# Kernel tuning notes

Hardware: AMD Instinct MI355X
Metric: run time of the kernel (lower is better)

## Reference

```python
import jax, jax.numpy as jnp
import numpy as np

N, DEG = 20000, 16
E = N * DEG
D_IN, D_HID, D_OUT, L = 1024, 512, 128, 3


def setup_inputs() -> dict:
    key = jax.random.key(0)
    ks = jax.random.split(key, 16)
    scale = 0.02
    X = jax.random.normal(ks[0], (N, D_IN), dtype=jnp.float32)
    senders = jax.random.randint(ks[1], (E,), 0, N)
    receivers = jnp.repeat(jnp.arange(N), DEG)  # sorted, every node has DEG neighbors
    inp = {"X": X, "senders": senders, "receivers": receivers}
    ki = 2
    for l in range(L):
        din = D_IN >> l
        dh = D_HID >> l
        inp[f"lw{l}"] = jax.random.normal(ks[ki], (2 * din, dh), jnp.float32) * scale; ki += 1
        inp[f"lb{l}"] = jnp.zeros((dh,), jnp.float32)
        inp[f"aw{l}"] = jax.random.normal(ks[ki], (din, dh), jnp.float32) * scale; ki += 1
        inp[f"aq{l}"] = jax.random.normal(ks[ki], (dh,), jnp.float32) * scale; ki += 1
    inp["ow"] = jax.random.normal(ks[ki], (D_HID >> (L - 1), D_OUT), jnp.float32) * scale
    inp["ob"] = jnp.zeros((D_OUT,), jnp.float32)
    return inp


def _attend(h, senders, receivers, aw, aq):
    # scores depend only on the neighbor (sender) embedding: q @ relu(W h_j)
    logits = jnp.einsum('nh,h->n', jax.nn.relu(h @ aw), aq)            # [N]
    el = logits[senders]                                               # [E]
    m = jax.ops.segment_max(el, receivers, num_segments=N)            # per-receiver max
    w = jnp.exp(el - m[receivers])                                     # [E]
    denom = jax.ops.segment_sum(w, receivers, num_segments=N)         # [N]
    msg = jax.ops.segment_sum(w[:, None] * h[senders], receivers, num_segments=N)  # [N,D]
    return msg / denom[:, None]


def reference(X, senders, receivers,
              lw0, lb0, aw0, aq0,
              lw1, lb1, aw1, aq1,
              lw2, lb2, aw2, aq2,
              ow, ob):
    params = [(lw0, lb0, aw0, aq0), (lw1, lb1, aw1, aq1), (lw2, lb2, aw2, aq2)]
    h = X
    for lw, lb, aw, aq in params:
        hN = _attend(h, senders, receivers, aw, aq)
        h = jax.nn.relu(jnp.concatenate([h, hN], axis=1) @ lw + lb)
    return h[14] @ ow + ob
```

## Files before the change

kernel.cpp:

```cpp
#include <hip/hip_runtime.h>
#include <math.h>

typedef unsigned short ushort_t;
typedef __attribute__((ext_vector_type(8))) short short8;
typedef __attribute__((ext_vector_type(4))) float f32x4;

#define NN    20000
#define DEG   16
constexpr int MAXL2 = 1 + DEG;
constexpr int MAXL1 = MAXL2 + MAXL2*DEG;
constexpr int MAXL0 = MAXL1*DEG;
constexpr int L0PAD = 73 * 64;
constexpr int NWBLK = 512;

__device__ __forceinline__ ushort_t f2bf(float f) {
    unsigned u = __float_as_uint(f);
    return (ushort_t)((u + 0x7FFFu + ((u >> 16) & 1u)) >> 16);
}

__global__ __launch_bounds__(256)
void k_frontier(const int* __restrict__ senders,
                int* list2, int* inv2, int* list1, int* inv1,
                int* list0, int* inv0, int* cnts, float4* zp, int n4) {
    int t = threadIdx.x;
    if (blockIdx.x > 0) {
        int i = (blockIdx.x - 1) * 256 + t;
        if (i < n4) zp[i] = make_float4(0.f, 0.f, 0.f, 0.f);
        return;
    }
    __shared__ unsigned bm[625];
    __shared__ int cnt;
    auto clear = [&]() { for (int i = t; i < 625; i += 256) bm[i] = 0u; if (t == 0) cnt = 0; };
    auto tryadd = [&](int node, int* list, int* inv) {
        unsigned bit = 1u << (node & 31);
        unsigned old = atomicOr(&bm[node >> 5], bit);
        if (!(old & bit)) { int p = atomicAdd(&cnt, 1); list[p] = node; inv[node] = p; }
    };
    clear(); __syncthreads();
    if (t < 17) { int node = (t < 16) ? senders[14 * DEG + t] : 14; tryadd(node, list2, inv2); }
    __syncthreads();
    int c2 = cnt; if (t == 0) cnts[2] = c2;
    __syncthreads(); clear(); __syncthreads();
    for (int i = t; i < c2 * 17; i += 256) {
        int r = i / 17, k = i - 17 * r;
        int node = (k < 16) ? senders[list2[r] * DEG + k] : list2[r];
        tryadd(node, list1, inv1);
    }
    __syncthreads();
    int c1 = cnt; if (t == 0) cnts[1] = c1;
    __syncthreads(); clear(); __syncthreads();
    for (int i = t; i < c1 * 16; i += 256) {
        int r = i >> 4, k = i & 15;
        tryadd(senders[list1[r] * DEG + k], list0, inv0);
    }
    __syncthreads();
    if (t == 0) cnts[0] = cnt;
}

__global__ __launch_bounds__(256)
void k_prep(const float* __restrict__ W, ushort_t* __restrict__ WT,
            const float* __restrict__ X, const int* __restrict__ list0,
            const int* __restrict__ cnt0, ushort_t* __restrict__ Xg) {
    int t = threadIdx.x;
    if (blockIdx.x < NWBLK) {
        __shared__ float tile[32][33];
        int b = blockIdx.x;
        int bx = b & 15, by = b >> 4;
        int i0 = t >> 3, j0 = (t & 7) * 4;
        int k = by * 32 + i0, n0 = bx * 32;
        float4 v = *(const float4*)(W + (size_t)k * 512 + n0 + j0);
        tile[i0][j0] = v.x; tile[i0][j0 + 1] = v.y; tile[i0][j0 + 2] = v.z; tile[i0][j0 + 3] = v.w;
        __syncthreads();
        int n = n0 + i0, kc = j0;
        ushort_t* p = WT + (size_t)n * 1024 + by * 32 + kc;
        p[0] = f2bf(tile[kc][i0]); p[1] = f2bf(tile[kc + 1][i0]);
        p[2] = f2bf(tile[kc + 2][i0]); p[3] = f2bf(tile[kc + 3][i0]);
    } else {
        int r = blockIdx.x - NWBLK;
        int rc = *cnt0;
        ushort_t o0 = 0, o1 = 0, o2 = 0, o3 = 0;
        if (r < rc) {
            float4 v = *(const float4*)(X + (size_t)list0[r] * 1024 + t * 4);
            o0 = f2bf(v.x); o1 = f2bf(v.y); o2 = f2bf(v.z); o3 = f2bf(v.w);
        }
        ushort_t* p = Xg + (size_t)r * 1024 + t * 4;
        p[0] = o0; p[1] = o1; p[2] = o2; p[3] = o3;
    }
}

__global__ __launch_bounds__(256)
void k_logits_mfma(const ushort_t* __restrict__ Xg,
                   const ushort_t* __restrict__ WT,
                   const float* __restrict__ aq, float* __restrict__ lgc,
                   const int* __restrict__ cnt, int K, int KS) {
    __shared__ short As[64 * 40];
    __shared__ short Bs[64 * 40];
    int rcnt = *cnt;
    int row0 = blockIdx.x * 64;
    if (row0 >= rcnt) return;
    int col0 = blockIdx.y * 64;
    int kbeg = blockIdx.z * KS, kend = kbeg + KS;
    int t = threadIdx.x;
    int w = t >> 6, lane = t & 63;

    int sr = t >> 2, sk = (t & 3) * 8;
    const ushort_t* ap = Xg + (size_t)(row0 + sr) * K + sk;
    const ushort_t* bp = WT + (size_t)(col0 + sr) * K + sk;

    int fm = lane & 15, fq = lane >> 4;
    const short* arow = As + (w * 16 + fm) * 40 + fq * 8;
    const short* brow = Bs + fm * 40 + fq * 8;

    f32x4 acc0 = {0.f,0.f,0.f,0.f}, acc1 = {0.f,0.f,0.f,0.f};
    f32x4 acc2 = {0.f,0.f,0.f,0.f}, acc3 = {0.f,0.f,0.f,0.f};

    short8 pa = *(const short8*)(ap + kbeg);
    short8 pb = *(const short8*)(bp + kbeg);
    for (int k0 = kbeg; k0 < kend; k0 += 32) {
        *(short8*)(As + sr * 40 + sk) = pa;
        *(short8*)(Bs + sr * 40 + sk) = pb;
        __syncthreads();
        if (k0 + 32 < kend) {
            pa = *(const short8*)(ap + k0 + 32);
            pb = *(const short8*)(bp + k0 + 32);
        }
        short8 af = *(const short8*)arow;
        short8 b0 = *(const short8*)(brow);
        short8 b1 = *(const short8*)(brow + 16 * 40);
        short8 b2 = *(const short8*)(brow + 32 * 40);
        short8 b3 = *(const short8*)(brow + 48 * 40);
        acc0 = __builtin_amdgcn_mfma_f32_16x16x32_bf16(af, b0, acc0, 0, 0, 0);
        acc1 = __builtin_amdgcn_mfma_f32_16x16x32_bf16(af, b1, acc1, 0, 0, 0);
        acc2 = __builtin_amdgcn_mfma_f32_16x16x32_bf16(af, b2, acc2, 0, 0, 0);
        acc3 = __builtin_amdgcn_mfma_f32_16x16x32_bf16(af, b3, acc3, 0, 0, 0);
        __syncthreads();
    }

    float aqv0 = aq[col0 + fm], aqv1 = aq[col0 + 16 + fm];
    float aqv2 = aq[col0 + 32 + fm], aqv3 = aq[col0 + 48 + fm];
#pragma unroll
    for (int r = 0; r < 4; r++) {
        float v = fmaxf(acc0[r], 0.f) * aqv0 + fmaxf(acc1[r], 0.f) * aqv1
                + fmaxf(acc2[r], 0.f) * aqv2 + fmaxf(acc3[r], 0.f) * aqv3;
#pragma unroll
        for (int off = 1; off < 16; off <<= 1) v += __shfl_xor(v, off);
        if (fm == 0) atomicAdd(&lgc[row0 + w * 16 + fq * 4 + r], v);
    }
}

__global__ __launch_bounds__(256)
void k_matmul(const float* __restrict__ A1, const float* __restrict__ A2,
              const int* __restrict__ list, const int* __restrict__ inv,
              const float* __restrict__ B, const float* __restrict__ aq,
              float* __restrict__ C, const int* __restrict__ cnt,
              int amode, int omode, int K1, int K2, int NC, int KS) {
    __shared__ float As[32][68];
    __shared__ float Bs[32][64];
    __shared__ float rowsum[64];

    int rcnt = *cnt;
    int row0 = blockIdx.x * 64;
    if (row0 >= rcnt) return;
    int col0 = blockIdx.y * 64;
    int K = K1 + K2;
    int kbeg = blockIdx.z * KS;
    int kend = kbeg + KS; if (kend > K) kend = K;

    int t = threadIdx.x;
    int ty = t >> 4, tx = t & 15;
    int lr = t >> 2, kaoff = (t & 3) * 4;
    int grow = row0 + lr;
    bool rowValid = grow < rcnt;
    const float* rp1 = A1;
    const float* rp2 = A2;
    if (rowValid) {
        int hrow;
        if (amode == 0) hrow = grow;
        else { int node = list[grow]; hrow = (amode == 2) ? inv[node] : node; }
        rp1 = A1 + (size_t)hrow * K1;
        rp2 = A2 + (size_t)grow * K2;
    }
    const float* Bp = B + col0;
    int bidx0 = t, bidx1 = t + 256;

    auto loadA = [&](int k) -> float4 {
        if (!rowValid) return make_float4(0.f, 0.f, 0.f, 0.f);
        const float* src = (k < K1) ? (rp1 + k) : (rp2 + (k - K1));
        return *(const float4*)src;
    };
    auto loadB = [&](int idx, int k0) -> float4 {
        int row = idx >> 4, c4 = (idx & 15) * 4;
        return *(const float4*)(Bp + (size_t)(k0 + row) * NC + c4);
    };

    float4 pa0 = loadA(kbeg + kaoff);
    float4 pa1 = loadA(kbeg + kaoff + 16);
    float4 pb0 = loadB(bidx0, kbeg);
    float4 pb1 = loadB(bidx1, kbeg);

    float acc[4][4] = {};
    for (int k0 = kbeg; k0 < kend; k0 += 32) {
        As[kaoff + 0][lr] = pa0.x; As[kaoff + 1][lr] = pa0.y;
        As[kaoff + 2][lr] = pa0.z; As[kaoff + 3][lr] = pa0.w;
        As[kaoff + 16][lr] = pa1.x; As[kaoff + 17][lr] = pa1.y;
        As[kaoff + 18][lr] = pa1.z; As[kaoff + 19][lr] = pa1.w;
        *(float4*)&Bs[bidx0 >> 4][(bidx0 & 15) * 4] = pb0;
        *(float4*)&Bs[bidx1 >> 4][(bidx1 & 15) * 4] = pb1;
        __syncthreads();
        if (k0 + 32 < kend) {
            pa0 = loadA(k0 + 32 + kaoff);
            pa1 = loadA(k0 + 32 + kaoff + 16);
            pb0 = loadB(bidx0, k0 + 32);
            pb1 = loadB(bidx1, k0 + 32);
        }
#pragma unroll
        for (int kk = 0; kk < 32; kk++) {
            float4 a4 = *(const float4*)&As[kk][ty * 4];
            float4 b4 = *(const float4*)&Bs[kk][tx * 4];
            float a[4] = {a4.x, a4.y, a4.z, a4.w};
            float b[4] = {b4.x, b4.y, b4.z, b4.w};
#pragma unroll
            for (int i = 0; i < 4; i++)
#pragma unroll
                for (int j = 0; j < 4; j++) acc[i][j] += a[i] * b[j];
        }
        __syncthreads();
    }

    if (omode == 0) {
#pragma unroll
        for (int i = 0; i < 4; i++) {
            int r = row0 + ty * 4 + i;
            if (r < rcnt) {
                float* Crow = C + (size_t)r * NC + col0 + tx * 4;
#pragma unroll
                for (int j = 0; j < 4; j++) atomicAdd(&Crow[j], acc[i][j]);
            }
        }
    } else {
        if (t < 64) rowsum[t] = 0.f;
        __syncthreads();
        float aqv[4];
#pragma unroll
        for (int j = 0; j < 4; j++) aqv[j] = aq[col0 + tx * 4 + j];
#pragma unroll
        for (int i = 0; i < 4; i++) {
            float s = 0.f;
#pragma unroll
            for (int j = 0; j < 4; j++) {
                float v = acc[i][j];
                v = v > 0.f ? v : 0.f;
                s += v * aqv[j];
            }
            atomicAdd(&rowsum[ty * 4 + i], s);
        }
        __syncthreads();
        if (t < 64) {
            int r = row0 + t;
            if (r < rcnt) atomicAdd(&C[r], rowsum[t]);
        }
    }
}

__global__ void k_bias_relu(const float* __restrict__ C, const float* __restrict__ b,
                            float* __restrict__ H, const int* __restrict__ cnt, int ncShift) {
    int rcnt = *cnt;
    int NC = 1 << ncShift;
    int e = blockIdx.x * 256 + threadIdx.x;
    int r = e >> ncShift;
    if (r >= rcnt) return;
    int c = e & (NC - 1);
    float v = C[(size_t)r * NC + c] + b[c];
    H[(size_t)r * NC + c] = v > 0.f ? v : 0.f;
}

__global__ __launch_bounds__(256)
void k_agg(const float* __restrict__ Hsrc, const int* __restrict__ invH,
           const float* __restrict__ lgc, const int* __restrict__ invL,
           const int* __restrict__ senders,
           const int* __restrict__ listN, const int* __restrict__ cntN,
           float* __restrict__ hN, int din) {
    __shared__ int   s_row[DEG];
    __shared__ float s_w[DEG];
    __shared__ float s_scale;
    int b = blockIdx.x;
    if (b >= *cntN) return;
    int n = listN[b];
    int t = threadIdx.x;
    if (t < DEG) {
        int s = senders[n * DEG + t];
        s_row[t] = invH ? invH[s] : s;
        s_w[t] = lgc[invL ? invL[s] : s];
    }
    __syncthreads();
    if (t == 0) {
        float m = -1e30f;
        for (int k = 0; k < DEG; k++) m = fmaxf(m, s_w[k]);
        float d = 0.f;
        for (int k = 0; k < DEG; k++) { float w = expf(s_w[k] - m); s_w[k] = w; d += w; }
        s_scale = 1.f / d;
    }
    __syncthreads();
    float scale = s_scale;
    for (int dI = t; dI < din; dI += 256) {
        float acc = 0.f;
#pragma unroll
        for (int k = 0; k < DEG; k++)
            acc += s_w[k] * Hsrc[(size_t)s_row[k] * din + dI];
        hN[(size_t)b * din + dI] = acc * scale;
    }
}

__global__ __launch_bounds__(256)
void k_layer2(const float* __restrict__ h2c, const int* __restrict__ inv2,
              const int* __restrict__ senders,
              const float* __restrict__ aw2, const float* __restrict__ aq2,
              const float* __restrict__ lw2, const float* __restrict__ lb2,
              const float* __restrict__ ow, const float* __restrict__ ob,
              const int* __restrict__ cnt2, float* __restrict__ out) {
    __shared__ float h2s[17][256];
    __shared__ float pl[17][128];
    __shared__ float lg[17];
    __shared__ float wgt[16];
    __shared__ int   srow[16];
    __shared__ int   iv14s;
    __shared__ float hcat[512];
    __shared__ float h3[128];
    int t = threadIdx.x;
    int rc = *cnt2;
    for (int i = t; i < 17 * 256; i += 256) {
        int r = i >> 8, c = i & 255;
        h2s[r][c] = (r < rc) ? h2c[r * 256 + c] : 0.f;
    }
    if (t < 17) lg[t] = 0.f;
    if (t == 0) iv14s = inv2[14];
    __syncthreads();

    int c = t & 127, h = t >> 7;
    float acc[17];
#pragma unroll
    for (int i = 0; i < 17; i++) acc[i] = 0.f;
    for (int k4 = h * 32; k4 < h * 32 + 32; k4++) {
        int k = k4 * 4;
        float w0 = aw2[(size_t)k * 128 + c];
        float w1 = aw2[(size_t)(k + 1) * 128 + c];
        float w2 = aw2[(size_t)(k + 2) * 128 + c];
        float w3 = aw2[(size_t)(k + 3) * 128 + c];
#pragma unroll
        for (int r = 0; r < 17; r++) {
            float4 hv = *(const float4*)&h2s[r][k4 * 4];
            acc[r] += hv.x * w0 + hv.y * w1 + hv.z * w2 + hv.w * w3;
        }
    }
    if (h == 1) {
#pragma unroll
        for (int r = 0; r < 17; r++) pl[r][c] = acc[r];
    }
    __syncthreads();
    if (h == 0) {
        float aqv = aq2[c];
#pragma unroll
        for (int r = 0; r < 17; r++) {
            float v = acc[r] + pl[r][c];
            v = (v > 0.f ? v : 0.f) * aqv;
#pragma unroll
            for (int off = 1; off < 64; off <<= 1) v += __shfl_xor(v, off);
            if ((t & 63) == 0) atomicAdd(&lg[r], v);
        }
    }
    __syncthreads();
    if (t == 0) {
        float m = -1e30f; float l[16];
#pragma unroll
        for (int k = 0; k < 16; k++) {
            int s = senders[14 * DEG + k];
            int r = inv2[s];
            srow[k] = r; l[k] = lg[r];
            m = fmaxf(m, l[k]);
        }
        float d = 0.f;
#pragma unroll
        for (int k = 0; k < 16; k++) { float w = expf(l[k] - m); wgt[k] = w; d += w; }
        float invd = 1.f / d;
#pragma unroll
        for (int k = 0; k < 16; k++) wgt[k] *= invd;
    }
    __syncthreads();
    {
        float a = 0.f;
        int cc = t & 255;
        if (t < 256) {
#pragma unroll
            for (int k = 0; k < 16; k++) a += wgt[k] * h2s[srow[k]][cc];
            hcat[256 + cc] = a;
            hcat[cc] = h2s[iv14s][cc];
        }
    }
    __syncthreads();
    if (t < 128) {
        float a = lb2[t];
        for (int k = 0; k < 512; k++) a += hcat[k] * lw2[(size_t)k * 128 + t];
        h3[t] = a > 0.f ? a : 0.f;
    }
    __syncthreads();
    if (t < 128) {
        float a = ob[t];
        for (int k = 0; k < 128; k++) a += h3[k] * ow[(size_t)k * 128 + t];
        out[t] = a;
    }
}

extern "C" void kernel_launch(void* const* d_in, const int* in_sizes, int n_in,
                              void* d_out, int out_size, void* d_ws, size_t ws_size,
                              hipStream_t stream) {
    const float* X       = (const float*)d_in[0];
    const int*   senders = (const int*)d_in[1];
    const float* lw0 = (const float*)d_in[3];
    const float* lb0 = (const float*)d_in[4];
    const float* aw0 = (const float*)d_in[5];
    const float* aq0 = (const float*)d_in[6];
    const float* lw1 = (const float*)d_in[7];
    const float* lb1 = (const float*)d_in[8];
    const float* aw1 = (const float*)d_in[9];
    const float* aq1 = (const float*)d_in[10];
    const float* lw2 = (const float*)d_in[11];
    const float* lb2 = (const float*)d_in[12];
    const float* aw2 = (const float*)d_in[13];
    const float* aq2 = (const float*)d_in[14];
    const float* owp = (const float*)d_in[15];
    const float* obp = (const float*)d_in[16];
    float* out = (float*)d_out;

    char* ws = (char*)d_ws;
    size_t off = 0;
    auto alloc = [&](size_t nbytes) -> void* {
        void* p = ws + off;
        off += (nbytes + 255) & ~(size_t)255;
        return p;
    };
    float* lgc0 = (float*)alloc(L0PAD * 4);
    float* lgc1 = (float*)alloc(MAXL1 * 4);
    float* C0   = (float*)alloc((size_t)MAXL1 * 512 * 4);
    float* C1   = (float*)alloc((size_t)MAXL2 * 256 * 4);
    size_t zero_end = off;
    int* inv0  = (int*)alloc(NN * 4);
    int* inv1  = (int*)alloc(NN * 4);
    int* inv2  = (int*)alloc(NN * 4);
    int* list0 = (int*)alloc(L0PAD * 4);
    int* list1 = (int*)alloc(MAXL1 * 4);
    int* list2 = (int*)alloc(MAXL2 * 4);
    int* cnts  = (int*)alloc(4 * 4);
    ushort_t* Xg  = (ushort_t*)alloc((size_t)L0PAD * 1024 * 2);
    ushort_t* awT = (ushort_t*)alloc((size_t)512 * 1024 * 2);
    float* hN0c = (float*)alloc((size_t)MAXL1 * 1024 * 4);
    float* h1c  = (float*)alloc((size_t)MAXL1 * 512 * 4);
    float* hN1c = (float*)alloc((size_t)MAXL2 * 512 * 4);
    float* h2c  = (float*)alloc((size_t)MAXL2 * 256 * 4);
    (void)in_sizes; (void)n_in; (void)out_size; (void)ws_size;

    int nz4 = (int)(zero_end / 16);
    int nzb = (nz4 + 255) / 256;

    hipLaunchKernelGGL(k_frontier, dim3(1 + nzb), dim3(256), 0, stream,
                       senders, list2, inv2, list1, inv1, list0, inv0, cnts,
                       (float4*)ws, nz4);
    hipLaunchKernelGGL(k_prep, dim3(NWBLK + L0PAD), dim3(256), 0, stream,
                       aw0, awT, X, list0, cnts + 0, Xg);

    hipLaunchKernelGGL(k_logits_mfma, dim3(73, 512 / 64, 2), dim3(256), 0, stream,
                       Xg, awT, aq0, lgc0, cnts + 0, 1024, 512);
    hipLaunchKernelGGL(k_agg, dim3(MAXL1), dim3(256), 0, stream,
                       X, (const int*)nullptr, lgc0, inv0, senders, list1, cnts + 1, hN0c, 1024);
    hipLaunchKernelGGL(k_matmul, dim3((MAXL1 + 63) / 64, 512 / 64, 8), dim3(256), 0, stream,
                       X, hN0c, list1, (int*)nullptr, lw0, aq0, C0, cnts + 1,
                       1, 0, 1024, 1024, 512, 256);
    hipLaunchKernelGGL(k_bias_relu, dim3((MAXL1 * 512 + 255) / 256), dim3(256), 0, stream,
                       C0, lb0, h1c, cnts + 1, 9);

    hipLaunchKernelGGL(k_matmul, dim3((MAXL1 + 63) / 64, 256 / 64, 2), dim3(256), 0, stream,
                       h1c, h1c, list1, (int*)nullptr, aw1, aq1, lgc1, cnts + 1,
                       0, 1, 512, 0, 256, 256);
    hipLaunchKernelGGL(k_agg, dim3(MAXL2), dim3(256), 0, stream,
                       h1c, inv1, lgc1, inv1, senders, list2, cnts + 2, hN1c, 512);
    hipLaunchKernelGGL(k_matmul, dim3(1, 256 / 64, 8), dim3(256), 0, stream,
                       h1c, hN1c, list2, inv1, lw1, aq1, C1, cnts + 2,
                       2, 0, 512, 512, 256, 128);
    hipLaunchKernelGGL(k_bias_relu, dim3((MAXL2 * 256 + 255) / 256), dim3(256), 0, stream,
                       C1, lb1, h2c, cnts + 2, 8);

    hipLaunchKernelGGL(k_layer2, dim3(1), dim3(256), 0, stream,
                       h2c, inv2, senders, aw2, aq2, lw2, lb2, owp, obp, cnts + 2, out);
}
```

Measured before the change: 292.4 us.

## Replace single-block final layer with generic matmul/agg kernels and drop split-K

Replaces the monolithic one-block layer-2 kernel with the existing k_matmul and k_agg kernels, using a one-node list for the output row, plus a small k_out kernel for the output projection. It also removes split-K from the layer-0 logits MFMA kernel and from the layer-1 logits matmul. The intent is to spread the final-layer work over more blocks and to avoid the atomic accumulation of split-K on the logits. In exchange it adds three more kernel launches and gives the logits kernels fewer blocks.

Measured after the change: 284.1 us. -2.8%, faster.

```diff
diff --git a/kernel.cpp b/kernel.cpp
--- a/kernel.cpp
+++ b/kernel.cpp
@@ -21,7 +21,7 @@
 __global__ __launch_bounds__(256)
 void k_frontier(const int* __restrict__ senders,
                 int* list2, int* inv2, int* list1, int* inv1,
-                int* list0, int* inv0, int* cnts, float4* zp, int n4) {
+                int* list0, int* inv0, int* list3, int* cnts, float4* zp, int n4) {
     int t = threadIdx.x;
     if (blockIdx.x > 0) {
         int i = (blockIdx.x - 1) * 256 + t;
@@ -54,7 +54,7 @@
         tryadd(senders[list1[r] * DEG + k], list0, inv0);
     }
     __syncthreads();
-    if (t == 0) cnts[0] = cnt;
+    if (t == 0) { cnts[0] = cnt; cnts[3] = 1; list3[0] = 14; }
 }
 
 __global__ __launch_bounds__(256)
@@ -92,14 +92,13 @@
 void k_logits_mfma(const ushort_t* __restrict__ Xg,
                    const ushort_t* __restrict__ WT,
                    const float* __restrict__ aq, float* __restrict__ lgc,
-                   const int* __restrict__ cnt, int K, int KS) {
+                   const int* __restrict__ cnt, int K) {
     __shared__ short As[64 * 40];
     __shared__ short Bs[64 * 40];
     int rcnt = *cnt;
     int row0 = blockIdx.x * 64;
     if (row0 >= rcnt) return;
     int col0 = blockIdx.y * 64;
-    int kbeg = blockIdx.z * KS, kend = kbeg + KS;
     int t = threadIdx.x;
     int w = t >> 6, lane = t & 63;
 
@@ -114,13 +113,13 @@
     f32x4 acc0 = {0.f,0.f,0.f,0.f}, acc1 = {0.f,0.f,0.f,0.f};
     f32x4 acc2 = {0.f,0.f,0.f,0.f}, acc3 = {0.f,0.f,0.f,0.f};
 
-    short8 pa = *(const short8*)(ap + kbeg);
-    short8 pb = *(const short8*)(bp + kbeg);
-    for (int k0 = kbeg; k0 < kend; k0 += 32) {
+    short8 pa = *(const short8*)(ap);
+    short8 pb = *(const short8*)(bp);
+    for (int k0 = 0; k0 < K; k0 += 32) {
         *(short8*)(As + sr * 40 + sk) = pa;
         *(short8*)(Bs + sr * 40 + sk) = pb;
         __syncthreads();
-        if (k0 + 32 < kend) {
+        if (k0 + 32 < K) {
             pa = *(const short8*)(ap + k0 + 32);
             pb = *(const short8*)(bp + k0 + 32);
         }
@@ -311,103 +310,21 @@
     }
 }
 
-__global__ __launch_bounds__(256)
-void k_layer2(const float* __restrict__ h2c, const int* __restrict__ inv2,
-              const int* __restrict__ senders,
-              const float* __restrict__ aw2, const float* __restrict__ aq2,
-              const float* __restrict__ lw2, const float* __restrict__ lb2,
-              const float* __restrict__ ow, const float* __restrict__ ob,
-              const int* __restrict__ cnt2, float* __restrict__ out) {
-    __shared__ float h2s[17][256];
-    __shared__ float pl[17][128];
-    __shared__ float lg[17];
-    __shared__ float wgt[16];
-    __shared__ int   srow[16];
-    __shared__ int   iv14s;
-    __shared__ float hcat[512];
-    __shared__ float h3[128];
-    int t = threadIdx.x;
-    int rc = *cnt2;
-    for (int i = t; i < 17 * 256; i += 256) {
-        int r = i >> 8, c = i & 255;
-        h2s[r][c] = (r < rc) ? h2c[r * 256 + c] : 0.f;
-    }
-    if (t < 17) lg[t] = 0.f;
-    if (t == 0) iv14s = inv2[14];
-    __syncthreads();
-
-    int c = t & 127, h = t >> 7;
-    float acc[17];
-#pragma unroll
-    for (int i = 0; i < 17; i++) acc[i] = 0.f;
-    for (int k4 = h * 32; k4 < h * 32 + 32; k4++) {
-        int k = k4 * 4;
-        float w0 = aw2[(size_t)k * 128 + c];
-        float w1 = aw2[(size_t)(k + 1) * 128 + c];
-        float w2 = aw2[(size_t)(k + 2) * 128 + c];
-        float w3 = aw2[(size_t)(k + 3) * 128 + c];
-#pragma unroll
-        for (int r = 0; r < 17; r++) {
-            float4 hv = *(const float4*)&h2s[r][k4 * 4];
-            acc[r] += hv.x * w0 + hv.y * w1 + hv.z * w2 + hv.w * w3;
-        }
-    }
-    if (h == 1) {
-#pragma unroll
-        for (int r = 0; r < 17; r++) pl[r][c] = acc[r];
-    }
-    __syncthreads();
-    if (h == 0) {
-        float aqv = aq2[c];
-#pragma unroll
-        for (int r = 0; r < 17; r++) {
-            float v = acc[r] + pl[r][c];
-            v = (v > 0.f ? v : 0.f) * aqv;
-#pragma unroll
-            for (int off = 1; off < 64; off <<= 1) v += __shfl_xor(v, off);
-            if ((t & 63) == 0) atomicAdd(&lg[r], v);
-        }
-    }
-    __syncthreads();
-    if (t == 0) {
-        float m = -1e30f; float l[16];
-#pragma unroll
-        for (int k = 0; k < 16; k++) {
-            int s = senders[14 * DEG + k];
-            int r = inv2[s];
-            srow[k] = r; l[k] = lg[r];
-            m = fmaxf(m, l[k]);
-        }
-        float d = 0.f;
-#pragma unroll
-        for (int k = 0; k < 16; k++) { float w = expf(l[k] - m); wgt[k] = w; d += w; }
-        float invd = 1.f / d;
-#pragma unroll
-        for (int k = 0; k < 16; k++) wgt[k] *= invd;
-    }
-    __syncthreads();
-    {
-        float a = 0.f;
-        int cc = t & 255;
-        if (t < 256) {
-#pragma unroll
-            for (int k = 0; k < 16; k++) a += wgt[k] * h2s[srow[k]][cc];
-            hcat[256 + cc] = a;
-            hcat[cc] = h2s[iv14s][cc];
-        }
-    }
-    __syncthreads();
-    if (t < 128) {
-        float a = lb2[t];
-        for (int k = 0; k < 512; k++) a += hcat[k] * lw2[(size_t)k * 128 + t];
-        h3[t] = a > 0.f ? a : 0.f;
-    }
-    __syncthreads();
-    if (t < 128) {
-        float a = ob[t];
-        for (int k = 0; k < 128; k++) a += h3[k] * ow[(size_t)k * 128 + t];
-        out[t] = a;
-    }
+__global__ __launch_bounds__(512)
+void k_out(const float* __restrict__ C2, const float* __restrict__ lb2,
+           const float* __restrict__ OW, const float* __restrict__ OB,
+           float* __restrict__ out) {
+    __shared__ float h3s[128];
+    __shared__ float part[4][128];
+    int t = threadIdx.x;
+    if (t < 128) { float v = C2[t] + lb2[t]; h3s[t] = v > 0.f ? v : 0.f; }
+    __syncthreads();
+    int j = t & 127, s = t >> 7;
+    float a = 0.f;
+    for (int k = s * 32; k < s * 32 + 32; k++) a += h3s[k] * OW[(size_t)k * 128 + j];
+    part[s][j] = a;
+    __syncthreads();
+    if (t < 128) out[t] = OB[t] + part[0][t] + part[1][t] + part[2][t] + part[3][t];
 }
 
 extern "C" void kernel_launch(void* const* d_in, const int* in_sizes, int n_in,
@@ -440,8 +357,10 @@
     };
     float* lgc0 = (float*)alloc(L0PAD * 4);
     float* lgc1 = (float*)alloc(MAXL1 * 4);
+    float* lgc2 = (float*)alloc(MAXL2 * 4);
     float* C0   = (float*)alloc((size_t)MAXL1 * 512 * 4);
     float* C1   = (float*)alloc((size_t)MAXL2 * 256 * 4);
+    float* C2   = (float*)alloc(128 * 4);
     size_t zero_end = off;
     int* inv0  = (int*)alloc(NN * 4);
     int* inv1  = (int*)alloc(NN * 4);
@@ -449,6 +368,7 @@
     int* list0 = (int*)alloc(L0PAD * 4);
     int* list1 = (int*)alloc(MAXL1 * 4);
     int* list2 = (int*)alloc(MAXL2 * 4);
+    int* list3 = (int*)alloc(4);
     int* cnts  = (int*)alloc(4 * 4);
     ushort_t* Xg  = (ushort_t*)alloc((size_t)L0PAD * 1024 * 2);
     ushort_t* awT = (ushort_t*)alloc((size_t)512 * 1024 * 2);
@@ -456,19 +376,20 @@
     float* h1c  = (float*)alloc((size_t)MAXL1 * 512 * 4);
     float* hN1c = (float*)alloc((size_t)MAXL2 * 512 * 4);
     float* h2c  = (float*)alloc((size_t)MAXL2 * 256 * 4);
+    float* hN2c = (float*)alloc(256 * 4);
     (void)in_sizes; (void)n_in; (void)out_size; (void)ws_size;
 
     int nz4 = (int)(zero_end / 16);
     int nzb = (nz4 + 255) / 256;
 
     hipLaunchKernelGGL(k_frontier, dim3(1 + nzb), dim3(256), 0, stream,
-                       senders, list2, inv2, list1, inv1, list0, inv0, cnts,
+                       senders, list2, inv2, list1, inv1, list0, inv0, list3, cnts,
                        (float4*)ws, nz4);
     hipLaunchKernelGGL(k_prep, dim3(NWBLK + L0PAD), dim3(256), 0, stream,
                        aw0, awT, X, list0, cnts + 0, Xg);
 
-    hipLaunchKernelGGL(k_logits_mfma, dim3(73, 512 / 64, 2), dim3(256), 0, stream,
-                       Xg, awT, aq0, lgc0, cnts + 0, 1024, 512);
+    hipLaunchKernelGGL(k_logits_mfma, dim3(73, 512 / 64, 1), dim3(256), 0, stream,
+                       Xg, awT, aq0, lgc0, cnts + 0, 1024);
     hipLaunchKernelGGL(k_agg, dim3(MAXL1), dim3(256), 0, stream,
                        X, (const int*)nullptr, lgc0, inv0, senders, list1, cnts + 1, hN0c, 1024);
     hipLaunchKernelGGL(k_matmul, dim3((MAXL1 + 63) / 64, 512 / 64, 8), dim3(256), 0, stream,
@@ -477,9 +398,9 @@
     hipLaunchKernelGGL(k_bias_relu, dim3((MAXL1 * 512 + 255) / 256), dim3(256), 0, stream,
                        C0, lb0, h1c, cnts + 1, 9);
 
-    hipLaunchKernelGGL(k_matmul, dim3((MAXL1 + 63) / 64, 256 / 64, 2), dim3(256), 0, stream,
+    hipLaunchKernelGGL(k_matmul, dim3((MAXL1 + 63) / 64, 256 / 64, 1), dim3(256), 0, stream,
                        h1c, h1c, list1, (int*)nullptr, aw1, aq1, lgc1, cnts + 1,
-                       0, 1, 512, 0, 256, 256);
+                       0, 1, 512, 0, 256, 512);
     hipLaunchKernelGGL(k_agg, dim3(MAXL2), dim3(256), 0, stream,
                        h1c, inv1, lgc1, inv1, senders, list2, cnts + 2, hN1c, 512);
     hipLaunchKernelGGL(k_matmul, dim3(1, 256 / 64, 8), dim3(256), 0, stream,
@@ -488,6 +409,13 @@
     hipLaunchKernelGGL(k_bias_relu, dim3((MAXL2 * 256 + 255) / 256), dim3(256), 0, stream,
                        C1, lb1, h2c, cnts + 2, 8);
 
-    hipLaunchKernelGGL(k_layer2, dim3(1), dim3(256), 0, stream,
-                       h2c, inv2, senders, aw2, aq2, lw2, lb2, owp, obp, cnts + 2, out);
-}
+    hipLaunchKernelGGL(k_matmul, dim3(1, 128 / 64, 1), dim3(256), 0, stream,
+                       h2c, h2c, list2, (int*)nullptr, aw2, aq2, lgc2, cnts + 2,
+                       0, 1, 256, 0, 128, 256);
+    hipLaunchKernelGGL(k_agg, dim3(1), dim3(256), 0, stream,
+                       h2c, inv2, lgc2, inv2, senders, list3, cnts + 3, hN2c, 256);
+    hipLaunchKernelGGL(k_matmul, dim3(1, 128 / 64, 4), dim3(256), 0, stream,
+                       h2c, hN2c, list3, inv2, lw2, aq2, C2, cnts + 3,
+                       2, 0, 256, 256, 128, 128);
+    hipLaunchKernelGGL(k_out, dim3(1), dim3(512), 0, stream, C2, lb2, owp, obp, out);
+}
```
